# Performance work log

Hardware: AMD Instinct MI355X
Metric: run time of the kernel (lower is better)

The kernel has to match this reference:

```python
import jax, jax.numpy as jnp
import numpy as np

N, IN_DIM, H, D = 4096, 512, 4, 64


def setup_inputs() -> dict:
    key = jax.random.key(0)
    k1, k2, k3, k4 = jax.random.split(key, 4)
    features = jax.random.normal(k1, (N, IN_DIM), dtype=jnp.float32)
    adjacency = jax.random.randint(k2, (N, N), 0, 2, dtype=jnp.int32)
    weights = jax.random.normal(k3, (IN_DIM, D * H), dtype=jnp.float32) * (1.414 / np.sqrt(IN_DIM))
    attention = jax.random.normal(k4, (1, H, 2 * D), dtype=jnp.float32) * 0.1
    bias = jnp.zeros((D * H,), dtype=jnp.float32)
    return {"features": features, "adjacency": adjacency, "weights": weights,
            "attention": attention, "bias": bias}


def reference(features, adjacency, weights, attention, bias):
    n = features.shape[0]
    h = (features @ weights).reshape(n, H, D)  # [N, H, D]
    # e[i,j,h] = leakyrelu(a1_h . h_i + a2_h . h_j)  (concat-attention decomposed)
    a1 = attention[0, :, :D]   # [H, D]
    a2 = attention[0, :, D:]   # [H, D]
    s1 = jnp.einsum('nhd,hd->nh', h, a1)  # [N, H]
    s2 = jnp.einsum('nhd,hd->nh', h, a2)  # [N, H]
    e = jax.nn.leaky_relu(s1[:, None, :] + s2[None, :, :], negative_slope=0.2)  # [N, N, H]
    masked = jnp.where(adjacency[:, :, None] > 0, e, jnp.float32(-9e15))
    attn = jax.nn.softmax(masked, axis=1)  # softmax over neighbors j (dim=1)
    out = jnp.einsum('ijh,jhd->ihd', attn, h).reshape(n, H * D)
    return out + bias
```

## Files before the change

kernel.cpp:

```cpp
#include <hip/hip_runtime.h>
#include <hip/hip_bf16.h>

#define N_NODES 4096
#define IN_DIMC 512
#define NHEADS 4
#define DHEAD 64
#define OUT_COLS 256
#define HPB (N_NODES * DHEAD * 2)

typedef __attribute__((ext_vector_type(8))) short short8;
typedef __attribute__((ext_vector_type(4))) float f32x4;

__device__ __forceinline__ short bf16b(float x) {
    return __builtin_bit_cast(short, __float2bfloat16(x));
}
__device__ __forceinline__ void gload16(const void* g, void* l) {
    __builtin_amdgcn_global_load_lds((const __attribute__((address_space(1))) void*)g,
                                     (__attribute__((address_space(3))) void*)l,
                                     16, 0, 0);
}
__device__ __forceinline__ void gload4(const void* g, void* l) {
    __builtin_amdgcn_global_load_lds((const __attribute__((address_space(1))) void*)g,
                                     (__attribute__((address_space(3))) void*)l,
                                     4, 0, 0);
}

__global__ __launch_bounds__(256) void k_prep2(
    const float* __restrict__ A, const float* __restrict__ W,
    const float* __restrict__ att, const int* __restrict__ adj,
    char* __restrict__ hP, float* __restrict__ E1, float* __restrict__ F1,
    float* __restrict__ E2, float* __restrict__ F2,
    unsigned* __restrict__ bits32)
{
    const int t = (int)threadIdx.x;
    if (blockIdx.x >= 512) {
        const int pb = (int)blockIdx.x - 512;
        const int i = pb * 4 + (t >> 6);
        const int lane = t & 63;
        const int* arow = adj + (size_t)i * N_NODES;
        #pragma unroll 2
        for (int it = 0; it < 16; ++it) {
            const int c = it * 4;
            const int a0 = arow[(c + 0) * 64 + lane];
            const int a1 = arow[(c + 1) * 64 + lane];
            const int a2 = arow[(c + 2) * 64 + lane];
            const int a3 = arow[(c + 3) * 64 + lane];
            const unsigned long long m0 = __ballot(a0 != 0);
            const unsigned long long m1 = __ballot(a1 != 0);
            const unsigned long long m2 = __ballot(a2 != 0);
            const unsigned long long m3 = __ballot(a3 != 0);
            if (lane == 0) {
                bits32[(size_t)(2 * c + 0) * N_NODES + i] = (unsigned)m0;
                bits32[(size_t)(2 * c + 1) * N_NODES + i] = (unsigned)(m0 >> 32);
                bits32[(size_t)(2 * c + 2) * N_NODES + i] = (unsigned)m1;
                bits32[(size_t)(2 * c + 3) * N_NODES + i] = (unsigned)(m1 >> 32);
                bits32[(size_t)(2 * c + 4) * N_NODES + i] = (unsigned)m2;
                bits32[(size_t)(2 * c + 5) * N_NODES + i] = (unsigned)(m2 >> 32);
                bits32[(size_t)(2 * c + 6) * N_NODES + i] = (unsigned)m3;
                bits32[(size_t)(2 * c + 7) * N_NODES + i] = (unsigned)(m3 >> 32);
            }
        }
        return;
    }
    __shared__ float As[32][36];
    __shared__ float Bs[32][68];
    __shared__ float ht[64][33];
    const int m0 = ((int)blockIdx.x & 127) * 32;
    const int head = (int)blockIdx.x >> 7;
    const int n0 = head * 64;
    const int tm = t & 7, tn = t >> 3;
    float acc[4][2] = {};
    for (int k0 = 0; k0 < IN_DIMC; k0 += 32) {
        {
            const int r = t >> 3, kc = (t & 7) << 2;
            float4 v0 = *(const float4*)(A + (size_t)(m0 + r) * IN_DIMC + k0 + kc);
            As[kc + 0][r] = v0.x; As[kc + 1][r] = v0.y; As[kc + 2][r] = v0.z; As[kc + 3][r] = v0.w;
            const int rb = t >> 4, nc = (t & 15) << 2;
            float4 w0 = *(const float4*)(W + (size_t)(k0 + rb) * OUT_COLS + n0 + nc);
            float4 w1 = *(const float4*)(W + (size_t)(k0 + rb + 16) * OUT_COLS + n0 + nc);
            *(float4*)&Bs[rb][nc] = w0;
            *(float4*)&Bs[rb + 16][nc] = w1;
        }
        __syncthreads();
        #pragma unroll
        for (int kk = 0; kk < 32; ++kk) {
            const f32x4 a = *(const f32x4*)&As[kk][tm << 2];
            const float b0 = Bs[kk][tn * 2], b1 = Bs[kk][tn * 2 + 1];
            #pragma unroll
            for (int i = 0; i < 4; ++i) {
                acc[i][0] = fmaf(a[i], b0, acc[i][0]);
                acc[i][1] = fmaf(a[i], b1, acc[i][1]);
            }
        }
        __syncthreads();
    }
    #pragma unroll
    for (int i = 0; i < 4; ++i) {
        ht[tn * 2 + 0][(tm << 2) + i] = acc[i][0];
        ht[tn * 2 + 1][(tm << 2) + i] = acc[i][1];
    }
    __syncthreads();
    {
        const int d = t >> 2, qq = t & 3;
        short8 hv;
        #pragma unroll
        for (int k = 0; k < 8; ++k) hv[k] = bf16b(ht[d][qq * 8 + k]);
        const size_t off16 = ((size_t)(m0 >> 5) * 4 + (d >> 4)) * 64 + qq * 16 + (d & 15);
        *(short8*)(hP + (size_t)head * HPB + off16 * 16) = hv;
    }
    {
        const int r = t >> 3, part = t & 7;
        float p1 = 0.f, p2 = 0.f;
        #pragma unroll
        for (int dd = 0; dd < 8; ++dd) {
            const int d = part * 8 + dd;
            const float v = ht[d][r];
            p1 = fmaf(v, att[head * 128 + d], p1);
            p2 = fmaf(v, att[head * 128 + 64 + d], p2);
        }
        p1 += __shfl_xor(p1, 1); p1 += __shfl_xor(p1, 2); p1 += __shfl_xor(p1, 4);
        p2 += __shfl_xor(p2, 1); p2 += __shfl_xor(p2, 2); p2 += __shfl_xor(p2, 4);
        if (part == 0) {
            const int idx = head * N_NODES + m0 + r;
            E1[idx] = __expf(p1);
            F1[idx] = __expf(0.2f * p1);
            E2[idx] = __expf(p2);
            F2[idx] = __expf(0.2f * p2);
        }
    }
}

__global__ __launch_bounds__(512, 4) void k_gat(
    const unsigned* __restrict__ bits32, const char* __restrict__ hP,
    const float* __restrict__ E1, const float* __restrict__ F1,
    const float* __restrict__ E2, const float* __restrict__ F2,
    float* __restrict__ pA, float* __restrict__ pB,
    float* __restrict__ pC, float* __restrict__ pD, float* __restrict__ pDen)
{
    __shared__ __align__(16) char stage[8 * 9216];
    const int i0 = (int)blockIdx.x * 32;
    const int by = (int)blockIdx.y;
    const int t = (int)threadIdx.x;
    const int w = t >> 6, lane = t & 63, il = lane & 15, q = lane >> 4;
    const int head = w & 3, jseg = w >> 2;
    const int jbase = by * 1024 + jseg * 512;
    char* myst = stage + w * 9216;
    const char* hPh = hP + (size_t)head * HPB;
    const float* E2h = E2 + head * N_NODES;
    const float* F2h = F2 + head * N_NODES;
    const float e1a = E1[head * N_NODES + i0 + il];
    const float e1b = E1[head * N_NODES + i0 + 16 + il];
    const float f1a = F1[head * N_NODES + i0 + il];
    const float f1b = F1[head * N_NODES + i0 + 16 + il];
    f32x4 acc[4][2] = {};
    f32x4 accD[2] = {};
    short8 ones;
    #pragma unroll
    for (int e = 0; e < 8; ++e) ones[e] = (short)0x3F80;

    const int g0 = jbase >> 5;
    auto issue = [&](int bs, char* dst) {
        const char* hsrc = hPh + (size_t)(g0 + bs) * 4096;
        #pragma unroll
        for (int k = 0; k < 4; ++k)
            gload16(hsrc + k * 1024 + lane * 16, dst + k * 1024);
        if (lane < 32) {
            gload4(E2h + jbase + bs * 32 + lane, dst + 4096);
            gload4(F2h + jbase + bs * 32 + lane, dst + 4224);
            gload4((const char*)(bits32 + (size_t)(g0 + bs) * N_NODES + i0) + lane * 4,
                   dst + 4352);
        }
    };
    issue(0, myst);
    #pragma unroll 2
    for (int s = 0; s < 16; ++s) {
        if (s < 15) {
            issue(s + 1, myst + ((s + 1) & 1) * 4608);
            asm volatile("s_waitcnt vmcnt(7)" ::: "memory");
        } else {
            asm volatile("s_waitcnt vmcnt(0)" ::: "memory");
        }
        const char* base = myst + (s & 1) * 4608;
        const unsigned uA = *(const unsigned*)(base + 4352 + il * 4);
        const unsigned uB = *(const unsigned*)(base + 4352 + 64 + il * 4);
        const f32x4 ea = *(const f32x4*)(base + 4096 + q * 32);
        const f32x4 eb = *(const f32x4*)(base + 4096 + q * 32 + 16);
        const f32x4 fa = *(const f32x4*)(base + 4224 + q * 32);
        const f32x4 fb2 = *(const f32x4*)(base + 4224 + q * 32 + 16);
        const unsigned mA = (uA >> (q * 8)) & 0xffu;
        const unsigned mB = (uB >> (q * 8)) & 0xffu;
        short8 afA, afB;
        #pragma unroll
        for (int e = 0; e < 8; ++e) {
            const float Ev = (e < 4) ? ea[e] : eb[e - 4];
            const float Fv = (e < 4) ? fa[e] : fb2[e - 4];
            const float pa = fmaxf(e1a * Ev, f1a * Fv);
            const float pb = fmaxf(e1b * Ev, f1b * Fv);
            afA[e] = bf16b(((mA >> e) & 1u) ? pa : 0.f);
            afB[e] = bf16b(((mB >> e) & 1u) ? pb : 0.f);
        }
        #pragma unroll
        for (int dblk = 0; dblk < 4; ++dblk) {
            const short8 bfrag = *(const short8*)(base + dblk * 1024 + lane * 16);
            acc[dblk][0] = __builtin_amdgcn_mfma_f32_16x16x32_bf16(afA, bfrag, acc[dblk][0], 0, 0, 0);
            acc[dblk][1] = __builtin_amdgcn_mfma_f32_16x16x32_bf16(afB, bfrag, acc[dblk][1], 0, 0, 0);
        }
        accD[0] = __builtin_amdgcn_mfma_f32_16x16x32_bf16(afA, ones, accD[0], 0, 0, 0);
        accD[1] = __builtin_amdgcn_mfma_f32_16x16x32_bf16(afB, ones, accD[1], 0, 0, 0);
    }
    __syncthreads();
    float* ep = (float*)stage;
    if (jseg == 1) {
        float* dst = ep + (w - 4) * 2560;
        #pragma unroll
        for (int dblk = 0; dblk < 4; ++dblk)
            #pragma unroll
            for (int sub = 0; sub < 2; ++sub)
                #pragma unroll
                for (int r = 0; r < 4; ++r)
                    dst[(dblk * 8 + sub * 4 + r) * 64 + lane] = acc[dblk][sub][r];
        #pragma unroll
        for (int sub = 0; sub < 2; ++sub)
            #pragma unroll
            for (int r = 0; r < 4; ++r)
                dst[(32 + sub * 4 + r) * 64 + lane] = accD[sub][r];
    }
    __syncthreads();
    if (jseg == 0) {
        const float* src = ep + w * 2560;
        float* po = (by == 0) ? pA : (by == 1) ? pB : (by == 2) ? pC : pD;
        #pragma unroll
        for (int sub = 0; sub < 2; ++sub) {
            #pragma unroll
            for (int r = 0; r < 4; ++r) {
                const int row = i0 + sub * 16 + q * 4 + r;
                #pragma unroll
                for (int dblk = 0; dblk < 4; ++dblk) {
                    const float v = acc[dblk][sub][r] + src[(dblk * 8 + sub * 4 + r) * 64 + lane];
                    po[(size_t)row * OUT_COLS + head * DHEAD + dblk * 16 + il] = v;
                }
                if (il == 0) {
                    const float d = accD[sub][r] + src[(32 + sub * 4 + r) * 64 + lane];
                    pDen[by * (NHEADS * N_NODES) + head * N_NODES + row] = d;
                }
            }
        }
    }
}

__global__ __launch_bounds__(256) void k_fin(
    const float* __restrict__ pB, const float* __restrict__ pC,
    const float* __restrict__ pD, const float* __restrict__ pDen,
    const float* __restrict__ bias, float* __restrict__ outp)
{
    const int gid = (int)blockIdx.x * 256 + (int)threadIdx.x;
    const int i = gid >> 6;
    const int c4 = (gid & 63) << 2;
    const int head = c4 >> 6;
    const float4 v0 = *(const float4*)(outp + (size_t)i * OUT_COLS + c4);
    const float4 v1 = *(const float4*)(pB + (size_t)i * OUT_COLS + c4);
    const float4 v2 = *(const float4*)(pC + (size_t)i * OUT_COLS + c4);
    const float4 v3 = *(const float4*)(pD + (size_t)i * OUT_COLS + c4);
    const float d = pDen[head * N_NODES + i]
                  + pDen[1 * NHEADS * N_NODES + head * N_NODES + i]
                  + pDen[2 * NHEADS * N_NODES + head * N_NODES + i]
                  + pDen[3 * NHEADS * N_NODES + head * N_NODES + i];
    const float inv = 1.0f / d;
    const float4 bb = *(const float4*)(bias + c4);
    float4 r;
    r.x = (v0.x + v1.x + v2.x + v3.x) * inv + bb.x;
    r.y = (v0.y + v1.y + v2.y + v3.y) * inv + bb.y;
    r.z = (v0.z + v1.z + v2.z + v3.z) * inv + bb.z;
    r.w = (v0.w + v1.w + v2.w + v3.w) * inv + bb.w;
    *(float4*)(outp + (size_t)i * OUT_COLS + c4) = r;
}

extern "C" void kernel_launch(void* const* d_in, const int* in_sizes, int n_in,
                              void* d_out, int out_size, void* d_ws, size_t ws_size,
                              hipStream_t stream) {
    const float* features  = (const float*)d_in[0];
    const int*   adjacency = (const int*)d_in[1];
    const float* weights   = (const float*)d_in[2];
    const float* attention = (const float*)d_in[3];
    const float* bias      = (const float*)d_in[4];
    float* out = (float*)d_out;

    char* ws = (char*)d_ws;
    char*     hP     = ws;
    float*    E1     = (float*)(ws + 2u*1024*1024);
    float*    F1     = (float*)(ws + 2u*1024*1024 +  64u*1024);
    float*    E2     = (float*)(ws + 2u*1024*1024 + 128u*1024);
    float*    F2     = (float*)(ws + 2u*1024*1024 + 192u*1024);
    unsigned* bits32 = (unsigned*)(ws + 2u*1024*1024 + 256u*1024);
    float*    pB     = (float*)(ws + 4u*1024*1024 + 256u*1024);
    float*    pC     = (float*)(ws + 8u*1024*1024 + 256u*1024);
    float*    pD     = (float*)(ws + 12u*1024*1024 + 256u*1024);
    float*    pDen   = (float*)(ws + 16u*1024*1024 + 256u*1024);

    k_prep2<<<dim3(1536), 256, 0, stream>>>(features, weights, attention, adjacency,
                                            hP, E1, F1, E2, F2, bits32);
    k_gat<<<dim3(128, 4), 512, 0, stream>>>(bits32, hP, E1, F1, E2, F2,
                                            out , pB, pC, pD, pDen);
    k_fin<<<dim3(1024), 256, 0, stream>>>(pB, pC, pD, pDen, bias, out);
}
```

Baseline: 60.74 us.

## Double rows per GAT block and deepen LDS pipeline to three stages

Each k_gat block now covers 64 destination rows instead of 32, so every staged tile of h, E2/F2 and adjacency bits is reused by four MFMA row-subtiles instead of two. The load ring grows from double to triple buffering, with vmcnt waits adjusted to keep two tiles in flight. The grid halves to 256 blocks and launch bounds drop to 2 blocks per CU, so per-thread accumulators and LDS use double while fewer blocks run, which may leave CUs underused.

```diff
diff --git a/kernel.cpp b/kernel.cpp
--- a/kernel.cpp
+++ b/kernel.cpp
@@ -130,36 +130,39 @@
     }
 }
 
-__global__ __launch_bounds__(512, 4) void k_gat(
+__global__ __launch_bounds__(512, 2) void k_gat(
     const unsigned* __restrict__ bits32, const char* __restrict__ hP,
     const float* __restrict__ E1, const float* __restrict__ F1,
     const float* __restrict__ E2, const float* __restrict__ F2,
     float* __restrict__ pA, float* __restrict__ pB,
     float* __restrict__ pC, float* __restrict__ pD, float* __restrict__ pDen)
 {
-    __shared__ __align__(16) char stage[8 * 9216];
-    const int i0 = (int)blockIdx.x * 32;
+    __shared__ __align__(16) char stage[8 * 13824];
+    const int i0 = (int)blockIdx.x * 64;
     const int by = (int)blockIdx.y;
     const int t = (int)threadIdx.x;
     const int w = t >> 6, lane = t & 63, il = lane & 15, q = lane >> 4;
     const int head = w & 3, jseg = w >> 2;
     const int jbase = by * 1024 + jseg * 512;
-    char* myst = stage + w * 9216;
+    char* myst = stage + w * 13824;
     const char* hPh = hP + (size_t)head * HPB;
     const float* E2h = E2 + head * N_NODES;
     const float* F2h = F2 + head * N_NODES;
-    const float e1a = E1[head * N_NODES + i0 + il];
-    const float e1b = E1[head * N_NODES + i0 + 16 + il];
-    const float f1a = F1[head * N_NODES + i0 + il];
-    const float f1b = F1[head * N_NODES + i0 + 16 + il];
-    f32x4 acc[4][2] = {};
-    f32x4 accD[2] = {};
+    float e1[4], f1[4];
+    #pragma unroll
+    for (int sub = 0; sub < 4; ++sub) {
+        e1[sub] = E1[head * N_NODES + i0 + sub * 16 + il];
+        f1[sub] = F1[head * N_NODES + i0 + sub * 16 + il];
+    }
+    f32x4 acc[4][4] = {};
+    f32x4 accD[4] = {};
     short8 ones;
     #pragma unroll
     for (int e = 0; e < 8; ++e) ones[e] = (short)0x3F80;
 
     const int g0 = jbase >> 5;
-    auto issue = [&](int bs, char* dst) {
+    auto issue = [&](int bs) {
+        char* dst = myst + (bs % 3) * 4608;
         const char* hsrc = hPh + (size_t)(g0 + bs) * 4096;
         #pragma unroll
         for (int k = 0; k < 4; ++k)
@@ -167,80 +170,90 @@
         if (lane < 32) {
             gload4(E2h + jbase + bs * 32 + lane, dst + 4096);
             gload4(F2h + jbase + bs * 32 + lane, dst + 4224);
-            gload4((const char*)(bits32 + (size_t)(g0 + bs) * N_NODES + i0) + lane * 4,
-                   dst + 4352);
-        }
+        }
+        gload4((const char*)(bits32 + (size_t)(g0 + bs) * N_NODES + i0) + lane * 4,
+               dst + 4352);
     };
-    issue(0, myst);
-    #pragma unroll 2
+    issue(0);
+    issue(1);
     for (int s = 0; s < 16; ++s) {
-        if (s < 15) {
-            issue(s + 1, myst + ((s + 1) & 1) * 4608);
+        if (s < 14) {
+            issue(s + 2);
+            asm volatile("s_waitcnt vmcnt(14)" ::: "memory");
+        } else if (s == 14) {
             asm volatile("s_waitcnt vmcnt(7)" ::: "memory");
         } else {
             asm volatile("s_waitcnt vmcnt(0)" ::: "memory");
         }
-        const char* base = myst + (s & 1) * 4608;
-        const unsigned uA = *(const unsigned*)(base + 4352 + il * 4);
-        const unsigned uB = *(const unsigned*)(base + 4352 + 64 + il * 4);
-        const f32x4 ea = *(const f32x4*)(base + 4096 + q * 32);
-        const f32x4 eb = *(const f32x4*)(base + 4096 + q * 32 + 16);
-        const f32x4 fa = *(const f32x4*)(base + 4224 + q * 32);
+        const char* base = myst + (s % 3) * 4608;
+        const f32x4 ea  = *(const f32x4*)(base + 4096 + q * 32);
+        const f32x4 eb  = *(const f32x4*)(base + 4096 + q * 32 + 16);
+        const f32x4 fa  = *(const f32x4*)(base + 4224 + q * 32);
         const f32x4 fb2 = *(const f32x4*)(base + 4224 + q * 32 + 16);
-        const unsigned mA = (uA >> (q * 8)) & 0xffu;
-        const unsigned mB = (uB >> (q * 8)) & 0xffu;
-        short8 afA, afB;
+        unsigned um[4];
+        #pragma unroll
+        for (int sub = 0; sub < 4; ++sub)
+            um[sub] = (*(const unsigned*)(base + 4352 + (sub * 16 + il) * 4)
+                       >> (q * 8)) & 0xffu;
+        short8 af[4];
         #pragma unroll
         for (int e = 0; e < 8; ++e) {
             const float Ev = (e < 4) ? ea[e] : eb[e - 4];
             const float Fv = (e < 4) ? fa[e] : fb2[e - 4];
-            const float pa = fmaxf(e1a * Ev, f1a * Fv);
-            const float pb = fmaxf(e1b * Ev, f1b * Fv);
-            afA[e] = bf16b(((mA >> e) & 1u) ? pa : 0.f);
-            afB[e] = bf16b(((mB >> e) & 1u) ? pb : 0.f);
+            #pragma unroll
+            for (int sub = 0; sub < 4; ++sub) {
+                const float p = fmaxf(e1[sub] * Ev, f1[sub] * Fv);
+                af[sub][e] = bf16b(((um[sub] >> e) & 1u) ? p : 0.f);
+            }
         }
         #pragma unroll
         for (int dblk = 0; dblk < 4; ++dblk) {
             const short8 bfrag = *(const short8*)(base + dblk * 1024 + lane * 16);
-            acc[dblk][0] = __builtin_amdgcn_mfma_f32_16x16x32_bf16(afA, bfrag, acc[dblk][0], 0, 0, 0);
-            acc[dblk][1] = __builtin_amdgcn_mfma_f32_16x16x32_bf16(afB, bfrag, acc[dblk][1], 0, 0, 0);
-        }
-        accD[0] = __builtin_amdgcn_mfma_f32_16x16x32_bf16(afA, ones, accD[0], 0, 0, 0);
-        accD[1] = __builtin_amdgcn_mfma_f32_16x16x32_bf16(afB, ones, accD[1], 0, 0, 0);
+            #pragma unroll
+            for (int sub = 0; sub < 4; ++sub)
+                acc[dblk][sub] = __builtin_amdgcn_mfma_f32_16x16x32_bf16(
+                    af[sub], bfrag, acc[dblk][sub], 0, 0, 0);
+        }
+        #pragma unroll
+        for (int sub = 0; sub < 4; ++sub)
+            accD[sub] = __builtin_amdgcn_mfma_f32_16x16x32_bf16(
+                af[sub], ones, accD[sub], 0, 0, 0);
     }
     __syncthreads();
     float* ep = (float*)stage;
     if (jseg == 1) {
-        float* dst = ep + (w - 4) * 2560;
-        #pragma unroll
-        for (int dblk = 0; dblk < 4; ++dblk)
-            #pragma unroll
-            for (int sub = 0; sub < 2; ++sub)
+        float* dst = ep + (w - 4) * 4352;
+        #pragma unroll
+        for (int sub = 0; sub < 4; ++sub) {
+            #pragma unroll
+            for (int dblk = 0; dblk < 4; ++dblk)
                 #pragma unroll
                 for (int r = 0; r < 4; ++r)
-                    dst[(dblk * 8 + sub * 4 + r) * 64 + lane] = acc[dblk][sub][r];
-        #pragma unroll
-        for (int sub = 0; sub < 2; ++sub)
-            #pragma unroll
-            for (int r = 0; r < 4; ++r)
-                dst[(32 + sub * 4 + r) * 64 + lane] = accD[sub][r];
+                    dst[sub * 1088 + (dblk * 4 + r) * 64 + lane] = acc[dblk][sub][r];
+            if (il == 0) {
+                #pragma unroll
+                for (int r = 0; r < 4; ++r)
+                    dst[sub * 1088 + 1024 + q * 4 + r] = accD[sub][r];
+            }
+        }
     }
     __syncthreads();
     if (jseg == 0) {
-        const float* src = ep + w * 2560;
+        const float* src = ep + w * 4352;
         float* po = (by == 0) ? pA : (by == 1) ? pB : (by == 2) ? pC : pD;
         #pragma unroll
-        for (int sub = 0; sub < 2; ++sub) {
+        for (int sub = 0; sub < 4; ++sub) {
             #pragma unroll
             for (int r = 0; r < 4; ++r) {
                 const int row = i0 + sub * 16 + q * 4 + r;
                 #pragma unroll
                 for (int dblk = 0; dblk < 4; ++dblk) {
-                    const float v = acc[dblk][sub][r] + src[(dblk * 8 + sub * 4 + r) * 64 + lane];
+                    const float v = acc[dblk][sub][r]
+                                  + src[sub * 1088 + (dblk * 4 + r) * 64 + lane];
                     po[(size_t)row * OUT_COLS + head * DHEAD + dblk * 16 + il] = v;
                 }
                 if (il == 0) {
-                    const float d = accD[sub][r] + src[(32 + sub * 4 + r) * 64 + lane];
+                    const float d = accD[sub][r] + src[sub * 1088 + 1024 + q * 4 + r];
                     pDen[by * (NHEADS * N_NODES) + head * N_NODES + row] = d;
                 }
             }
@@ -299,7 +312,7 @@
 
     k_prep2<<<dim3(1536), 256, 0, stream>>>(features, weights, attention, adjacency,
                                             hP, E1, F1, E2, F2, bits32);
-    k_gat<<<dim3(128, 4), 512, 0, stream>>>(bits32, hP, E1, F1, E2, F2,
-                                            out , pB, pC, pD, pDen);
+    k_gat<<<dim3(64, 4), 512, 0, stream>>>(bits32, hP, E1, F1, E2, F2,
+                                           out , pB, pC, pD, pDen);
     k_fin<<<dim3(1024), 256, 0, stream>>>(pB, pC, pD, pDen, bias, out);
 }
```

Measured after the change: 61.98 us. +2.0%, slower.
